# Optimization experiments

Hardware: AMD Instinct MI355X
Metric: run time of the kernel (lower is better)

The kernel has to match this reference:

```python
import jax, jax.numpy as jnp
import numpy as np
import math

LMAX = 8  # even real SH up to degree 8 -> K = 45 basis functions
BVALS = np.array([1.0, 2.0, 3.0], dtype=np.float32)


def _assoc_legendre(x, lmax):
    # associated Legendre P_l^m(x) for 0<=m<=l<=lmax via standard recurrences
    P = {(0, 0): jnp.ones_like(x)}
    s = jnp.sqrt(jnp.clip(1.0 - x * x, 0.0, 1.0))
    for m in range(1, lmax + 1):
        P[(m, m)] = -(2 * m - 1) * s * P[(m - 1, m - 1)]
    for m in range(0, lmax):
        P[(m + 1, m)] = (2 * m + 1) * x * P[(m, m)]
    for m in range(0, lmax + 1):
        for l in range(m + 2, lmax + 1):
            P[(l, m)] = ((2 * l - 1) * x * P[(l - 1, m)] - (l + m - 1) * P[(l - 2, m)]) / (l - m)
    return P


def _sh_degrees(lmax):
    # FuncSpace.n : degree l of each basis function (even degrees only)
    return np.array([l for l in range(0, lmax + 1, 2) for m in range(-l, l + 1)])


def real_sh_basis(dirs):
    # FuncSpace.harmonic_expansion: (..., 3) directions -> (..., K) real symmetric SH
    d = dirs / jnp.linalg.norm(dirs, axis=-1, keepdims=True)
    x, y, z = d[..., 0], d[..., 1], d[..., 2]
    phi = jnp.arctan2(y, x)
    P = _assoc_legendre(z, LMAX)  # cos(theta) = z
    cols = []
    for l in range(0, LMAX + 1, 2):
        for m in range(-l, l + 1):
            ma = abs(m)
            nrm = math.sqrt((2 * l + 1) / (4 * math.pi) * math.factorial(l - ma) / math.factorial(l + ma))
            if m < 0:
                cols.append(math.sqrt(2.0) * nrm * jnp.sin(ma * phi) * P[(l, ma)])
            elif m == 0:
                cols.append(nrm * P[(l, 0)])
            else:
                cols.append(math.sqrt(2.0) * nrm * jnp.cos(m * phi) * P[(l, m)])
    return jnp.stack(cols, axis=-1)


def _legendre_poly(t, lmax):
    # Legendre polynomials P_l(t), l = 0..lmax, shape (lmax+1, T)
    Ps = [jnp.ones_like(t), t]
    for n in range(1, lmax):
        Ps.append(((2 * n + 1) * t * Ps[n] - n * Ps[n - 1]) / (n + 1))
    return jnp.stack(Ps[: lmax + 1], axis=0)


def setup_inputs() -> dict:
    key = jax.random.key(0)
    k1, k2, k3 = jax.random.split(key, 3)
    N, F = 8192, 3
    return {
        "directs": jax.random.normal(k1, (N, F, 3), dtype=jnp.float32),
        "weights": jax.random.uniform(k2, (N, F), dtype=jnp.float32),
        "shapes": jax.random.uniform(k3, (N, F, 4), dtype=jnp.float32),
        "num_t": 1000,
    }


def reference(directs, weights, shapes, num_t):
    degrees = _sh_degrees(LMAX)                                  # (K,)
    l_ks, l_k_idx = np.unique(degrees, return_inverse=True)      # unique even degrees + map to K
    b = jnp.asarray(BVALS)                                       # (B,)
    t = jnp.linspace(0.0, 1.0, num_t)                            # (T,)
    t2 = t * t
    D_a, D_epar, D_eperp, z = (shapes[..., i] for i in range(4))  # each (N, F)
    bD = b[None, None, :, None]                                  # (1,1,B,1)
    # StandardModel kernel evaluations, batched over samples/fibers/bvals: (N,F,B,T)
    kern = (z[..., None, None] * jnp.exp(-bD * D_a[..., None, None] * t2)
            + (1.0 - z[..., None, None]) * jnp.exp(-bD * D_eperp[..., None, None]
                                                   - bD * (D_epar - D_eperp)[..., None, None] * t2))
    # trapezoid weights matching torch.trapz(y, dx=1/num_t) exactly
    w = jnp.full((num_t,), 1.0 / num_t).at[0].set(0.5 / num_t).at[-1].set(0.5 / num_t)
    P = _legendre_poly(t, int(l_ks.max()))[np.asarray(l_ks)]     # (L,T) at unique degrees
    rho = jnp.einsum('nfbt,lt->nbfl', kern * w, P)               # (N,B,F,L) rho_k integrals
    eigen_values = rho[..., np.asarray(l_k_idx)]                 # (N,B,F,K) broadcast to basis fns
    ODFtensor = real_sh_basis(directs)                           # (N,F,K)
    Stensor = jnp.einsum('nf,nbfk,nfk->nbk', weights, eigen_values, ODFtensor)  # sum over fibers
    return Stensor, ODFtensor, eigen_values
```

## Files before the change

kernel.cpp:

```cpp
#include <hip/hip_runtime.h>
#include <math.h>

#define FF 3
#define BB 3
#define KK 45
#define VOX 8
#define TPB 256
#define NT 18
#define NFIB (VOX*FF)
#define NRHO (VOX*FF*BB)

constexpr double csqrt(double x) {
    double g = x > 1.0 ? x : 1.0;
    for (int i = 0; i < 64; ++i) g = 0.5 * (g + x / g);
    return g;
}

struct Tab { float d[5][NT]; };
constexpr Tab make_tab() {
    Tab t{};
    for (int li = 0; li < 5; ++li) {
        const int l = 2 * li;
        double kfact = 1.0;
        for (int k = 0; k < NT; ++k) {
            if (k > 0) kfact *= (double)k;
            double c = 0.0;
            if (2 * k >= l) {
                double num = 1.0, den = 1.0;
                for (int j = 0; j < l / 2; ++j)  num *= (double)(2 * k - 2 * j);
                for (int j = 0; j <= l / 2; ++j) den *= (double)(2 * k + 1 + 2 * j);
                c = num / den;
            }
            t.d[li][k] = (float)(((k & 1) ? -1.0 : 1.0) * c / kfact);
        }
    }
    return t;
}
static constexpr Tab HOST_TAB = make_tab();
__constant__ Tab TAB = HOST_TAB;

struct KTab {
    float nrm[KK];
    unsigned char lidx[KK];
    unsigned char ma[KK];
    unsigned char neg[KK];
};
constexpr KTab make_ktab() {
    KTab t{};
    int k = 0;
    for (int l = 0; l <= 8; l += 2) {
        for (int m = -l; m <= l; ++m, ++k) {
            const int ma = m < 0 ? -m : m;
            double prod = 1.0;
            for (int i = l - ma + 1; i <= l + ma; ++i) prod *= (double)i;
            double nrm = csqrt((double)(2 * l + 1) * 0.07957747154594767 / prod);
            if (m != 0) nrm *= csqrt(2.0);
            t.nrm[k]  = (float)nrm;
            t.lidx[k] = (unsigned char)(l / 2);
            t.ma[k]   = (unsigned char)ma;
            t.neg[k]  = (unsigned char)(m < 0 ? 1 : 0);
        }
    }
    return t;
}
static constexpr KTab HKT = make_ktab();

struct STab { unsigned short v[BB * KK]; };
constexpr STab make_stab() {
    STab t{};
    KTab kt = make_ktab();
    for (int r = 0; r < BB * KK; ++r) {
        const int bi = r / KK;
        const int k  = r % KK;
        t.v[r] = (unsigned short)((unsigned)(bi * 5 + kt.lidx[k]) | ((unsigned)k << 8));
    }
    return t;
}
static constexpr STab HOST_STAB = make_stab();
__constant__ STab TS = HOST_STAB;

__device__ __forceinline__ void eval_I(float a, float I[5]) {
    #pragma unroll
    for (int li = 0; li < 5; ++li) {
        float acc = TAB.d[li][NT - 1];
        #pragma unroll
        for (int k = NT - 2; k >= 0; --k)
            acc = fmaf(acc, a, TAB.d[li][k]);
        I[li] = acc;
    }
}

__global__ __launch_bounds__(TPB) void fused_sim_kernel(
    const float* __restrict__ directs,
    const float* __restrict__ weights,
    const float* __restrict__ shapes,
    const int*   __restrict__ num_t_p,
    float* __restrict__ outS,
    float* __restrict__ outODF,
    float* __restrict__ outEig,
    int N)
{
    const int n0  = blockIdx.x * VOX;
    const int tid = threadIdx.x;
    const bool full = (n0 + VOX <= N);

    __shared__ __align__(16) float sh_s[NFIB * KK];
    __shared__ __align__(16) float eig_s[VOX * BB * FF * KK];
    __shared__ __align__(16) float wrho_s[NRHO * 5];

    if (tid < NFIB) {
        const int f = tid % FF;
        const int n = n0 + tid / FF;
        if (n < N) {
            const float dx = directs[(n * FF + f) * 3 + 0];
            const float dy = directs[(n * FF + f) * 3 + 1];
            const float dz = directs[(n * FF + f) * 3 + 2];
            const float inv = 1.0f / sqrtf(dx * dx + dy * dy + dz * dz);
            const float x = dx * inv, y = dy * inv, z = dz * inv;
            float s2 = 1.0f - z * z;
            s2 = fminf(fmaxf(s2, 0.0f), 1.0f);
            const float s = sqrtf(s2);

            const float rxy2 = x * x + y * y;
            float cphi = 1.0f, sphi = 0.0f;
            if (rxy2 > 0.0f) {
                const float ir = 1.0f / sqrtf(rxy2);
                cphi = x * ir;
                sphi = y * ir;
            }

            float cmv[9], smv[9];
            float cm = 1.0f, sm = 0.0f;
            #pragma unroll
            for (int m = 0; m <= 8; ++m) {
                cmv[m] = cm;
                smv[m] = sm;
                const float cn = cm * cphi - sm * sphi;
                const float sn = sm * cphi + cm * sphi;
                cm = cn; sm = sn;
            }

            float Preg[25];
            float pmm = 1.0f;
            #pragma unroll
            for (int ma = 0; ma <= 8; ++ma) {
                if (ma > 0) pmm *= -(float)(2 * ma - 1) * s;
                if ((ma & 1) == 0)
                    Preg[(ma / 2) * (ma / 2) + ma] = pmm;
                float pa = pmm;
                float pb = (float)(2 * ma + 1) * z * pa;
                if (ma + 1 <= 8 && ((ma + 1) & 1) == 0)
                    Preg[((ma + 1) / 2) * ((ma + 1) / 2) + ma] = pb;
                #pragma unroll
                for (int ll = ma + 2; ll <= 8; ++ll) {
                    const float invd = 1.0f / (float)(ll - ma);
                    const float pn = ((float)(2 * ll - 1) * z * pb
                                      - (float)(ll + ma - 1) * pa) * invd;
                    pa = pb; pb = pn;
                    if ((ll & 1) == 0)
                        Preg[(ll / 2) * (ll / 2) + ma] = pn;
                }
            }

            float* shrow = sh_s + tid * KK;
            #pragma unroll
            for (int k = 0; k < KK; ++k) {
                const int   lidx = HKT.lidx[k];
                const int   ma   = HKT.ma[k];
                const float tr   = HKT.neg[k] ? smv[ma] : cmv[ma];
                shrow[k] = HKT.nrm[k] * tr * Preg[lidx * lidx + ma];
            }
        }
    }

    if (tid >= 64 && tid < 64 + NRHO) {
        const int w  = tid - 64;
        const int fi = w / BB;
        const int bi = w % BB;
        const int v  = fi / FF;
        const int f  = fi % FF;
        const int n  = n0 + v;
        if (n < N) {
            const float bval = (float)(bi + 1);

            const float4 sp4 = *(const float4*)(shapes + (size_t)(n * FF + f) * 4);
            const float D_a     = sp4.x;
            const float D_epar  = sp4.y;
            const float D_eperp = sp4.z;
            const float zf      = sp4.w;

            const float bA = bval * D_a;
            const float bE = bval * (D_epar - D_eperp);
            const float zc = (1.0f - zf) * __expf(-bval * D_eperp);

            const float T     = (float)num_t_p[0];
            const float h     = 1.0f / (T - 1.0f);
            const float scale = (T - 1.0f) / T;
            const float h212  = h * h * (1.0f / 12.0f);

            float IA[5], IE[5];
            eval_I(bA, IA);
            eval_I(bE, IE);
            const float eA = __expf(-bA);
            const float eE = __expf(-bE);

            float rho[5];
            #pragma unroll
            for (int li = 0; li < 5; ++li) {
                const int   l   = 2 * li;
                const float pl1 = 0.5f * (float)(l * (l + 1));
                const float QA = IA[li] + h212 * eA * (pl1 - 2.0f * bA);
                const float QE = IE[li] + h212 * eE * (pl1 - 2.0f * bE);
                rho[li] = scale * (zf * QA + zc * QE);
            }

            const float wt = weights[n * FF + f];
            #pragma unroll
            for (int li = 0; li < 5; ++li)
                wrho_s[w * 5 + li] = wt * rho[li];

            float* er = eig_s + (v * (BB * FF) + bi * FF + f) * KK;
            #pragma unroll
            for (int k = 0; k < KK; ++k)
                er[k] = rho[HKT.lidx[k]];
        }
    }

    __syncthreads();

    {
        float4* dst = (float4*)(outEig + (size_t)n0 * (BB * FF * KK));
        const float4* src = (const float4*)eig_s;
        if (full) {
            for (int q = tid; q < VOX * BB * FF * KK / 4; q += TPB)
                dst[q] = src[q];
        } else {
            for (int e = tid; e < VOX * BB * FF * KK; e += TPB)
                if (n0 + e / (BB * FF * KK) < N)
                    outEig[(size_t)n0 * (BB * FF * KK) + e] = eig_s[e];
        }
    }

    {
        float4* dst = (float4*)(outODF + (size_t)n0 * (FF * KK));
        const float4* src = (const float4*)sh_s;
        if (full) {
            for (int q = tid; q < VOX * FF * KK / 4; q += TPB)
                dst[q] = src[q];
        } else {
            for (int e = tid; e < VOX * FF * KK; e += TPB)
                if (n0 + e / (FF * KK) < N)
                    outODF[(size_t)n0 * (FF * KK) + e] = sh_s[e];
        }
    }

    {
        float4* dst = (float4*)(outS + (size_t)n0 * (BB * KK));
        for (int q = tid; q < VOX * BB * KK / 4; q += TPB) {
            const int e0 = 4 * q;
            int vv = (int)((unsigned)e0 / (unsigned)(BB * KK));
            int r  = e0 - vv * (BB * KK);
            const float* wrb = wrho_s + vv * (FF * BB * 5);
            const float* shb = sh_s   + vv * (FF * KK);
            float4 out;
            float* oc = &out.x;
            #pragma unroll
            for (int j = 0; j < 4; ++j) {
                if (r >= BB * KK) { r -= BB * KK; wrb += FF * BB * 5; shb += FF * KK; }
                const unsigned ts = TS.v[r];
                const float* wr = wrb + (ts & 0xffu);
                const float* sp = shb + (ts >> 8);
                float ssum = 0.0f;
                ssum = fmaf(wr[0],  sp[0],  ssum);
                ssum = fmaf(wr[15], sp[45], ssum);
                ssum = fmaf(wr[30], sp[90], ssum);
                oc[j] = ssum;
                ++r;
            }
            if (full) {
                dst[q] = out;
            } else {
                #pragma unroll
                for (int j = 0; j < 4; ++j) {
                    const int e = 4 * q + j;
                    if (n0 + e / (BB * KK) < N)
                        outS[(size_t)n0 * (BB * KK) + e] = oc[j];
                }
            }
        }
    }
}

extern "C" void kernel_launch(void* const* d_in, const int* in_sizes, int n_in,
                              void* d_out, int out_size, void* d_ws, size_t ws_size,
                              hipStream_t stream) {
    const float* directs = (const float*)d_in[0];
    const float* weights = (const float*)d_in[1];
    const float* shapes  = (const float*)d_in[2];
    const int*   num_t   = (const int*)d_in[3];

    const int N = in_sizes[0] / (FF * 3);

    float* outS   = (float*)d_out;
    float* outODF = outS + (size_t)N * BB * KK;
    float* outEig = outODF + (size_t)N * FF * KK;

    const int blocks = (N + VOX - 1) / VOX;
    fused_sim_kernel<<<blocks, TPB, 0, stream>>>(directs, weights, shapes, num_t,
                                                 outS, outODF, outEig, N);
}
```

Before: 68.57 us.

## Make each wavefront own its voxels and replace block barrier with wave sync

Each 64-lane wavefront now handles 4 voxels in its own LDS slice. Within a wave, some lanes compute the SH rows and others compute the rho values, so the block-wide __syncthreads is replaced by a wave barrier plus an LDS waitcnt. Blocks now cover 16 voxels with 4 waves, which removes cross-wave synchronisation and lets more of each wave's lanes do work in the compute phase. It depends on the wave size being 64 and on LDS visibility inside a wave being correct with only the wave barrier and waitcnt.

```diff
diff --git a/kernel.cpp b/kernel.cpp
--- a/kernel.cpp
+++ b/kernel.cpp
@@ -4,11 +4,16 @@
 #define FF 3
 #define BB 3
 #define KK 45
-#define VOX 8
-#define TPB 256
+#define WV 4
+#define WPB 4
+#define VOXB (WV*WPB)
+#define TPB (WPB*64)
 #define NT 18
-#define NFIB (VOX*FF)
-#define NRHO (VOX*FF*BB)
+
+#define EIG_OFF 0
+#define SH_OFF  1620
+#define WR_OFF  2160
+#define SLICE   2340
 
 constexpr double csqrt(double x) {
     double g = x > 1.0 ? x : 1.0;
@@ -100,17 +105,19 @@
     float* __restrict__ outEig,
     int N)
 {
-    const int n0  = blockIdx.x * VOX;
-    const int tid = threadIdx.x;
-    const bool full = (n0 + VOX <= N);
-
-    __shared__ __align__(16) float sh_s[NFIB * KK];
-    __shared__ __align__(16) float eig_s[VOX * BB * FF * KK];
-    __shared__ __align__(16) float wrho_s[NRHO * 5];
-
-    if (tid < NFIB) {
-        const int f = tid % FF;
-        const int n = n0 + tid / FF;
+    const int wave = threadIdx.x >> 6;
+    const int lane = threadIdx.x & 63;
+    const int n0w  = blockIdx.x * VOXB + wave * WV;
+    if (n0w >= N) return;
+    const bool fullw = (n0w + WV <= N);
+
+    __shared__ __align__(16) float lds[WPB][SLICE];
+    float* sl = lds[wave];
+
+    if (lane < WV * FF) {
+        const int v = lane / FF;
+        const int f = lane % FF;
+        const int n = n0w + v;
         if (n < N) {
             const float dx = directs[(n * FF + f) * 3 + 0];
             const float dy = directs[(n * FF + f) * 3 + 1];
@@ -162,7 +169,7 @@
                 }
             }
 
-            float* shrow = sh_s + tid * KK;
+            float* shrow = sl + SH_OFF + lane * KK;
             #pragma unroll
             for (int k = 0; k < KK; ++k) {
                 const int   lidx = HKT.lidx[k];
@@ -172,14 +179,12 @@
             }
         }
     }
-
-    if (tid >= 64 && tid < 64 + NRHO) {
-        const int w  = tid - 64;
-        const int fi = w / BB;
-        const int bi = w % BB;
-        const int v  = fi / FF;
-        const int f  = fi % FF;
-        const int n  = n0 + v;
+    else if (lane < WV * FF + WV * FF * BB) {
+        const int j  = lane - WV * FF;
+        const int v  = j / (FF * BB);
+        const int f  = (j / BB) % FF;
+        const int bi = j % BB;
+        const int n  = n0w + v;
         if (n < N) {
             const float bval = (float)(bi + 1);
 
@@ -215,77 +220,94 @@
             }
 
             const float wt = weights[n * FF + f];
+            float* wr = sl + WR_OFF + j * 5;
             #pragma unroll
             for (int li = 0; li < 5; ++li)
-                wrho_s[w * 5 + li] = wt * rho[li];
-
-            float* er = eig_s + (v * (BB * FF) + bi * FF + f) * KK;
+                wr[li] = wt * rho[li];
+
+            float* er = sl + EIG_OFF + v * (BB * FF * KK) + bi * (FF * KK) + f * KK;
             #pragma unroll
             for (int k = 0; k < KK; ++k)
                 er[k] = rho[HKT.lidx[k]];
         }
     }
 
-    __syncthreads();
-
-    {
-        float4* dst = (float4*)(outEig + (size_t)n0 * (BB * FF * KK));
-        const float4* src = (const float4*)eig_s;
-        if (full) {
-            for (int q = tid; q < VOX * BB * FF * KK / 4; q += TPB)
-                dst[q] = src[q];
-        } else {
-            for (int e = tid; e < VOX * BB * FF * KK; e += TPB)
-                if (n0 + e / (BB * FF * KK) < N)
-                    outEig[(size_t)n0 * (BB * FF * KK) + e] = eig_s[e];
-        }
-    }
-
-    {
-        float4* dst = (float4*)(outODF + (size_t)n0 * (FF * KK));
-        const float4* src = (const float4*)sh_s;
-        if (full) {
-            for (int q = tid; q < VOX * FF * KK / 4; q += TPB)
-                dst[q] = src[q];
-        } else {
-            for (int e = tid; e < VOX * FF * KK; e += TPB)
-                if (n0 + e / (FF * KK) < N)
-                    outODF[(size_t)n0 * (FF * KK) + e] = sh_s[e];
-        }
-    }
-
-    {
-        float4* dst = (float4*)(outS + (size_t)n0 * (BB * KK));
-        for (int q = tid; q < VOX * BB * KK / 4; q += TPB) {
-            const int e0 = 4 * q;
-            int vv = (int)((unsigned)e0 / (unsigned)(BB * KK));
-            int r  = e0 - vv * (BB * KK);
-            const float* wrb = wrho_s + vv * (FF * BB * 5);
-            const float* shb = sh_s   + vv * (FF * KK);
-            float4 out;
-            float* oc = &out.x;
-            #pragma unroll
-            for (int j = 0; j < 4; ++j) {
-                if (r >= BB * KK) { r -= BB * KK; wrb += FF * BB * 5; shb += FF * KK; }
+    __builtin_amdgcn_wave_barrier();
+    asm volatile("s_waitcnt lgkmcnt(0)" ::: "memory");
+    __builtin_amdgcn_wave_barrier();
+
+    if (fullw) {
+        {
+            float4* dst = (float4*)(outEig + (size_t)n0w * (BB * FF * KK));
+            const float4* src = (const float4*)(sl + EIG_OFF);
+            #pragma unroll
+            for (int it = 0; it < 7; ++it) {
+                const int q = lane + it * 64;
+                if (q < WV * BB * FF * KK / 4) dst[q] = src[q];
+            }
+        }
+        {
+            float4* dst = (float4*)(outODF + (size_t)n0w * (FF * KK));
+            const float4* src = (const float4*)(sl + SH_OFF);
+            #pragma unroll
+            for (int it = 0; it < 3; ++it) {
+                const int q = lane + it * 64;
+                if (q < WV * FF * KK / 4) dst[q] = src[q];
+            }
+        }
+        {
+            float4* dst = (float4*)(outS + (size_t)n0w * (BB * KK));
+            #pragma unroll
+            for (int it = 0; it < 3; ++it) {
+                const int q = lane + it * 64;
+                if (q < WV * BB * KK / 4) {
+                    const int e0 = 4 * q;
+                    const int vv = (int)((unsigned)e0 / (unsigned)(BB * KK));
+                    int r = e0 - vv * (BB * KK);
+                    const float* wrb = sl + WR_OFF + vv * (FF * BB * 5);
+                    const float* shb = sl + SH_OFF + vv * (FF * KK);
+                    float4 out;
+                    float* oc = &out.x;
+                    #pragma unroll
+                    for (int jj = 0; jj < 4; ++jj) {
+                        if (r >= BB * KK) {
+                            r -= BB * KK;
+                            wrb += FF * BB * 5;
+                            shb += FF * KK;
+                        }
+                        const unsigned ts = TS.v[r];
+                        const float* wp = wrb + (ts & 0xffu);
+                        const float* sp = shb + (ts >> 8);
+                        float ssum = 0.0f;
+                        ssum = fmaf(wp[0],  sp[0],  ssum);
+                        ssum = fmaf(wp[15], sp[45], ssum);
+                        ssum = fmaf(wp[30], sp[90], ssum);
+                        oc[jj] = ssum;
+                        ++r;
+                    }
+                    dst[q] = out;
+                }
+            }
+        }
+    } else {
+        for (int e = lane; e < WV * BB * FF * KK; e += 64)
+            if (n0w + e / (BB * FF * KK) < N)
+                outEig[(size_t)n0w * (BB * FF * KK) + e] = sl[EIG_OFF + e];
+        for (int e = lane; e < WV * FF * KK; e += 64)
+            if (n0w + e / (FF * KK) < N)
+                outODF[(size_t)n0w * (FF * KK) + e] = sl[SH_OFF + e];
+        for (int e = lane; e < WV * BB * KK; e += 64) {
+            const int vv = e / (BB * KK);
+            if (n0w + vv < N) {
+                const int r = e - vv * (BB * KK);
                 const unsigned ts = TS.v[r];
-                const float* wr = wrb + (ts & 0xffu);
-                const float* sp = shb + (ts >> 8);
+                const float* wp = sl + WR_OFF + vv * (FF * BB * 5) + (ts & 0xffu);
+                const float* sp = sl + SH_OFF + vv * (FF * KK) + (ts >> 8);
                 float ssum = 0.0f;
-                ssum = fmaf(wr[0],  sp[0],  ssum);
-                ssum = fmaf(wr[15], sp[45], ssum);
-                ssum = fmaf(wr[30], sp[90], ssum);
-                oc[j] = ssum;
-                ++r;
-            }
-            if (full) {
-                dst[q] = out;
-            } else {
-                #pragma unroll
-                for (int j = 0; j < 4; ++j) {
-                    const int e = 4 * q + j;
-                    if (n0 + e / (BB * KK) < N)
-                        outS[(size_t)n0 * (BB * KK) + e] = oc[j];
-                }
+                ssum = fmaf(wp[0],  sp[0],  ssum);
+                ssum = fmaf(wp[15], sp[45], ssum);
+                ssum = fmaf(wp[30], sp[90], ssum);
+                outS[(size_t)n0w * (BB * KK) + e] = ssum;
             }
         }
     }
@@ -305,7 +327,7 @@
     float* outODF = outS + (size_t)N * BB * KK;
     float* outEig = outODF + (size_t)N * FF * KK;
 
-    const int blocks = (N + VOX - 1) / VOX;
+    const int blocks = (N + VOXB - 1) / VOXB;
     fused_sim_kernel<<<blocks, TPB, 0, stream>>>(directs, weights, shapes, num_t,
                                                  outS, outODF, outEig, N);
 }
```

Measured after the change: 69.89 us. About the same (+1.9%).
